# Performance work log

Measured on AMD Instinct MI355X. Metric: run time of the kernel, lower is better.

Reference implementation:

```python
import jax, jax.numpy as jnp
import numpy as np

# Winograd F(2x2, 3x3) transform matrices, copied verbatim from the source
# (note: G[1,2] is 1.2 in the original code, not 0.5 -- replicated faithfully).
B_MAT = jnp.array([[1, 0, -1, 0], [0, 1, 1, 0], [0, -1, 1, 0], [0, 1, 0, -1]], dtype=jnp.float32)
G_MAT = jnp.array([[1.0, 0.0, 0.0], [0.5, 0.5, 1.2], [0.5, -0.5, 0.5], [0.0, 0.0, 1.0]], dtype=jnp.float32)
AT_MAT = jnp.array([[1, 1, 1, 0], [0, 1, -1, -1]], dtype=jnp.float32)


def setup_inputs() -> dict:
    key = jax.random.key(0)
    k1, k2 = jax.random.split(key)
    x = jax.random.normal(k1, (64, 64, 64, 64), dtype=jnp.float32)        # [B, C, H, W]
    filters = jax.random.normal(k2, (64, 64, 3, 3), dtype=jnp.float32)    # [F, C, 3, 3]
    return {"x": x, "filters": filters}


def winograd_forward(x, filters):
    bs, C, H, W = x.shape
    F = filters.shape[0]
    m, r = 2, 3
    alpha = m + r - 1          # 4
    over = r - 1               # 2 (tile stride)
    T = (W - alpha) // over + 1
    p = bs * T * T

    # U[f,c] = G @ g @ G^T   -> [F, C, 4, 4]
    U = jnp.einsum('ij,fcjk,lk->fcil', G_MAT, filters, G_MAT)

    # Extract all 4x4 input tiles with stride 2: [C, B, T, T, 4, 4]
    xt = jnp.transpose(x, (1, 0, 2, 3))                         # [C, B, H, W]
    win = (jnp.arange(T) * over)[:, None] + jnp.arange(alpha)[None, :]  # [T, 4]
    patches = xt[:, :, win[:, None, :, None], win[None, :, None, :]]    # [C,B,T,T,4,4]

    # V[c,b] = B^T @ d @ B, flattened with b = batch*T*T + row*T + col
    V = jnp.einsum('ji,cbtujk,kl->cbtuil', B_MAT, patches, B_MAT)
    V = V.reshape(C, p, alpha, alpha)

    # Faithful to the source bug: M[f, j] is only accumulated for j < T
    # (the loop is `for j in range(tiles)` instead of range(p)); rest stay zero.
    Mpart = jnp.einsum('fcab,cjab->fjab', U, V[:, :T])          # [F, T, 4, 4]
    M = jnp.zeros((F, p, alpha, alpha), x.dtype).at[:, :T].set(Mpart)

    # Faithful to the source: Y tile index b = f*T*T + k*T + l (depends on the
    # filter index, not the batch index), so every batch gets the same tiles.
    idx = (jnp.arange(F) * T * T)[:, None] + jnp.arange(T * T)[None, :]  # [F, T*T]
    Msel = M[jnp.arange(F)[:, None], idx]                        # [F, T*T, 4, 4]

    # Inverse transform: A^T @ M @ A -> [F, T*T, 2, 2]
    Yt = jnp.einsum('ij,ftjk,kl->ftil', AT_MAT, Msel, AT_MAT.T)
    out_h = H - r + 1
    Yt = Yt.reshape(F, T, T, m, m).transpose(0, 1, 3, 2, 4).reshape(F, T * m, T * m)
    # Original allocates Y as [F, B, H-2, H-2]; with H == W they match T*m.
    Y = jnp.broadcast_to(Yt[:, None, :, :], (F, bs, out_h, out_h))
    return jnp.transpose(Y, (1, 0, 2, 3))                        # [B, F, H-2, H-2]


def reference(x, filters):
    return winograd_forward(x, filters)
```

## Files before the change

### kernel.cpp

```cpp
#include <hip/hip_runtime.h>


__global__ void winograd_scatter(const float* __restrict__ x,
                                 const float* __restrict__ filters,
                                 float* __restrict__ out) {
    const int u = blockIdx.x;
    const int c = threadIdx.x;

    const float G[4][3]  = {{1.0f, 0.0f, 0.0f},
                            {0.5f, 0.5f, 1.2f},
                            {0.5f,-0.5f, 0.5f},
                            {0.0f, 0.0f, 1.0f}};
    const float Bm[4][4] = {{1.f, 0.f,-1.f, 0.f},
                            {0.f, 1.f, 1.f, 0.f},
                            {0.f,-1.f, 1.f, 0.f},
                            {0.f, 1.f, 0.f,-1.f}};

    float g[3][3];
#pragma unroll
    for (int j = 0; j < 3; ++j)
#pragma unroll
        for (int k = 0; k < 3; ++k)
            g[j][k] = filters[c * 9 + j * 3 + k];

    float t1[4][3];
#pragma unroll
    for (int i = 0; i < 4; ++i)
#pragma unroll
        for (int k = 0; k < 3; ++k) {
            float s = 0.f;
#pragma unroll
            for (int j = 0; j < 3; ++j) s += G[i][j] * g[j][k];
            t1[i][k] = s;
        }
    float U[4][4];
#pragma unroll
    for (int i = 0; i < 4; ++i)
#pragma unroll
        for (int l = 0; l < 4; ++l) {
            float s = 0.f;
#pragma unroll
            for (int k = 0; k < 3; ++k) s += t1[i][k] * G[l][k];
            U[i][l] = s;
        }

    float d[4][4];
#pragma unroll
    for (int j = 0; j < 4; ++j)
#pragma unroll
        for (int k = 0; k < 4; ++k)
            d[j][k] = x[c * 4096 + j * 64 + 2 * u + k];

    float t2[4][4];
#pragma unroll
    for (int i = 0; i < 4; ++i)
#pragma unroll
        for (int k = 0; k < 4; ++k) {
            float s = 0.f;
#pragma unroll
            for (int j = 0; j < 4; ++j) s += Bm[j][i] * d[j][k];
            t2[i][k] = s;
        }
    float V[4][4];
#pragma unroll
    for (int i = 0; i < 4; ++i)
#pragma unroll
        for (int l = 0; l < 4; ++l) {
            float s = 0.f;
#pragma unroll
            for (int k = 0; k < 4; ++k) s += t2[i][k] * Bm[k][l];
            V[i][l] = s;
        }

    __shared__ float red[16][64];
#pragma unroll
    for (int i = 0; i < 4; ++i)
#pragma unroll
        for (int l = 0; l < 4; ++l)
            red[i * 4 + l][c] = U[i][l] * V[i][l];
    __syncthreads();

    __shared__ float M[16];
    if (c < 16) {
        float s = 0.f;
        for (int t = 0; t < 64; ++t) s += red[c][t];
        M[c] = s;
    }
    __syncthreads();

    __shared__ float sY[4];
    if (c == 0) {
        const float AT[2][4] = {{1.f, 1.f, 1.f, 0.f},
                                {0.f, 1.f,-1.f,-1.f}};
        float t3[2][4];
#pragma unroll
        for (int i = 0; i < 2; ++i)
#pragma unroll
            for (int k = 0; k < 4; ++k) {
                float s = 0.f;
#pragma unroll
                for (int j = 0; j < 4; ++j) s += AT[i][j] * M[j * 4 + k];
                t3[i][k] = s;
            }
#pragma unroll
        for (int i = 0; i < 2; ++i)
#pragma unroll
            for (int l = 0; l < 2; ++l) {
                float s = 0.f;
#pragma unroll
                for (int k = 0; k < 4; ++k) s += t3[i][k] * AT[l][k];
                sY[i * 2 + l] = s;
            }
    }
    __syncthreads();

    const float2 r0 = make_float2(sY[0], sY[1]);
    const float2 r1 = make_float2(sY[2], sY[3]);
    float* base = out + (size_t)c * 246016 + 2 * u;
    *(float2*)(base)      = r0;
    *(float2*)(base + 62) = r1;
}

extern "C" void kernel_launch(void* const* d_in, const int* in_sizes, int n_in,
                              void* d_out, int out_size, void* d_ws, size_t ws_size,
                              hipStream_t stream) {
    const float* x       = (const float*)d_in[0];
    const float* filters = (const float*)d_in[1];
    float* out = (float*)d_out;

    hipMemsetAsync(d_out, 0, (size_t)out_size * sizeof(float), stream);
    winograd_scatter<<<31, 64, 0, stream>>>(x, filters, out);
}
```

Measured before the change: 105.6 us.

## Fuse output zero-fill into compute kernel, drop separate memset

```diff
diff --git a/kernel.cpp b/kernel.cpp
--- a/kernel.cpp
+++ b/kernel.cpp
@@ -1,95 +1,119 @@
 #include <hip/hip_runtime.h>
 
 
-__global__ void winograd_scatter(const float* __restrict__ x,
-                                 const float* __restrict__ filters,
-                                 float* __restrict__ out) {
+#define COMPUTE_BLOCKS 31
+#define FILL_BLOCKS    2048
+#define BLOCK          256
+#define N4             3936256
+#define BSTRIDE4       61504
+#define SKIP4          31
+
+__global__ __launch_bounds__(BLOCK)
+void winograd_fused(const float* __restrict__ x,
+                    const float* __restrict__ filters,
+                    float* __restrict__ out) {
+    const int tid = threadIdx.x;
+
+    if (blockIdx.x >= COMPUTE_BLOCKS) {
+        const int fb = (int)blockIdx.x - COMPUTE_BLOCKS;
+        const float4 z = make_float4(0.f, 0.f, 0.f, 0.f);
+        float4* __restrict__ o4 = (float4*)out;
+        for (int i = fb * BLOCK + tid; i < N4; i += FILL_BLOCKS * BLOCK) {
+            const int rem = i % BSTRIDE4;
+            if (rem >= SKIP4) o4[i] = z;
+        }
+        return;
+    }
+
     const int u = blockIdx.x;
-    const int c = threadIdx.x;
-
-    const float G[4][3]  = {{1.0f, 0.0f, 0.0f},
-                            {0.5f, 0.5f, 1.2f},
-                            {0.5f,-0.5f, 0.5f},
-                            {0.0f, 0.0f, 1.0f}};
-    const float Bm[4][4] = {{1.f, 0.f,-1.f, 0.f},
-                            {0.f, 1.f, 1.f, 0.f},
-                            {0.f,-1.f, 1.f, 0.f},
-                            {0.f, 1.f, 0.f,-1.f}};
-
-    float g[3][3];
-#pragma unroll
-    for (int j = 0; j < 3; ++j)
-#pragma unroll
-        for (int k = 0; k < 3; ++k)
-            g[j][k] = filters[c * 9 + j * 3 + k];
-
-    float t1[4][3];
-#pragma unroll
-    for (int i = 0; i < 4; ++i)
-#pragma unroll
-        for (int k = 0; k < 3; ++k) {
-            float s = 0.f;
-#pragma unroll
-            for (int j = 0; j < 3; ++j) s += G[i][j] * g[j][k];
-            t1[i][k] = s;
-        }
-    float U[4][4];
-#pragma unroll
-    for (int i = 0; i < 4; ++i)
-#pragma unroll
-        for (int l = 0; l < 4; ++l) {
-            float s = 0.f;
-#pragma unroll
-            for (int k = 0; k < 3; ++k) s += t1[i][k] * G[l][k];
-            U[i][l] = s;
-        }
-
-    float d[4][4];
-#pragma unroll
-    for (int j = 0; j < 4; ++j)
-#pragma unroll
-        for (int k = 0; k < 4; ++k)
-            d[j][k] = x[c * 4096 + j * 64 + 2 * u + k];
-
-    float t2[4][4];
-#pragma unroll
-    for (int i = 0; i < 4; ++i)
-#pragma unroll
-        for (int k = 0; k < 4; ++k) {
-            float s = 0.f;
-#pragma unroll
-            for (int j = 0; j < 4; ++j) s += Bm[j][i] * d[j][k];
-            t2[i][k] = s;
-        }
-    float V[4][4];
-#pragma unroll
-    for (int i = 0; i < 4; ++i)
-#pragma unroll
-        for (int l = 0; l < 4; ++l) {
-            float s = 0.f;
-#pragma unroll
-            for (int k = 0; k < 4; ++k) s += t2[i][k] * Bm[k][l];
-            V[i][l] = s;
-        }
+    const int c = tid & 63;
 
     __shared__ float red[16][64];
+    __shared__ float Msm[16];
+    __shared__ float sY[4];
+
+    if (tid < 64) {
+        const float G[4][3]  = {{1.0f, 0.0f, 0.0f},
+                                {0.5f, 0.5f, 1.2f},
+                                {0.5f,-0.5f, 0.5f},
+                                {0.0f, 0.0f, 1.0f}};
+        const float Bm[4][4] = {{1.f, 0.f,-1.f, 0.f},
+                                {0.f, 1.f, 1.f, 0.f},
+                                {0.f,-1.f, 1.f, 0.f},
+                                {0.f, 1.f, 0.f,-1.f}};
+
+        float g[3][3];
 #pragma unroll
-    for (int i = 0; i < 4; ++i)
+        for (int j = 0; j < 3; ++j)
 #pragma unroll
-        for (int l = 0; l < 4; ++l)
-            red[i * 4 + l][c] = U[i][l] * V[i][l];
-    __syncthreads();
+            for (int k = 0; k < 3; ++k)
+                g[j][k] = filters[c * 9 + j * 3 + k];
 
-    __shared__ float M[16];
-    if (c < 16) {
-        float s = 0.f;
-        for (int t = 0; t < 64; ++t) s += red[c][t];
-        M[c] = s;
+        float t1[4][3];
+#pragma unroll
+        for (int i = 0; i < 4; ++i)
+#pragma unroll
+            for (int k = 0; k < 3; ++k) {
+                float s = 0.f;
+#pragma unroll
+                for (int j = 0; j < 3; ++j) s += G[i][j] * g[j][k];
+                t1[i][k] = s;
+            }
+        float U[4][4];
+#pragma unroll
+        for (int i = 0; i < 4; ++i)
+#pragma unroll
+            for (int l = 0; l < 4; ++l) {
+                float s = 0.f;
+#pragma unroll
+                for (int k = 0; k < 3; ++k) s += t1[i][k] * G[l][k];
+                U[i][l] = s;
+            }
+
+        float d[4][4];
+#pragma unroll
+        for (int j = 0; j < 4; ++j)
+#pragma unroll
+            for (int k = 0; k < 4; ++k)
+                d[j][k] = x[c * 4096 + j * 64 + 2 * u + k];
+
+        float t2[4][4];
+#pragma unroll
+        for (int i = 0; i < 4; ++i)
+#pragma unroll
+            for (int k = 0; k < 4; ++k) {
+                float s = 0.f;
+#pragma unroll
+                for (int j = 0; j < 4; ++j) s += Bm[j][i] * d[j][k];
+                t2[i][k] = s;
+            }
+        float V[4][4];
+#pragma unroll
+        for (int i = 0; i < 4; ++i)
+#pragma unroll
+            for (int l = 0; l < 4; ++l) {
+                float s = 0.f;
+#pragma unroll
+                for (int k = 0; k < 4; ++k) s += t2[i][k] * Bm[k][l];
+                V[i][l] = s;
+            }
+
+#pragma unroll
+        for (int i = 0; i < 4; ++i)
+#pragma unroll
+            for (int l = 0; l < 4; ++l)
+                red[i * 4 + l][c] = U[i][l] * V[i][l];
     }
     __syncthreads();
 
-    __shared__ float sY[4];
-    if (c == 0) {
+    if (tid < 16) {
+        float s = 0.f;
+        for (int t = 0; t < 64; ++t) s += red[tid][t];
+        Msm[tid] = s;
+    }
+    __syncthreads();
+
+    if (tid == 0) {
         const float AT[2][4] = {{1.f, 1.f, 1.f, 0.f},
                                 {0.f, 1.f,-1.f,-1.f}};
         float t3[2][4];
@@ -99,7 +123,7 @@
             for (int k = 0; k < 4; ++k) {
                 float s = 0.f;
 #pragma unroll
-                for (int j = 0; j < 4; ++j) s += AT[i][j] * M[j * 4 + k];
+                for (int j = 0; j < 4; ++j) s += AT[i][j] * Msm[j * 4 + k];
                 t3[i][k] = s;
             }
 #pragma unroll
@@ -114,11 +138,13 @@
     }
     __syncthreads();
 
-    const float2 r0 = make_float2(sY[0], sY[1]);
-    const float2 r1 = make_float2(sY[2], sY[3]);
-    float* base = out + (size_t)c * 246016 + 2 * u;
-    *(float2*)(base)      = r0;
-    *(float2*)(base + 62) = r1;
+    if (tid < 64) {
+        const float2 r0 = make_float2(sY[0], sY[1]);
+        const float2 r1 = make_float2(sY[2], sY[3]);
+        float* base = out + (size_t)c * 246016 + 2 * u;
+        *(float2*)(base)      = r0;
+        *(float2*)(base + 62) = r1;
+    }
 }
 
 extern "C" void kernel_launch(void* const* d_in, const int* in_sizes, int n_in,
@@ -128,6 +154,5 @@
     const float* filters = (const float*)d_in[1];
     float* out = (float*)d_out;
 
-    hipMemsetAsync(d_out, 0, (size_t)out_size * sizeof(float), stream);
-    winograd_scatter<<<31, 64, 0, stream>>>(x, filters, out);
+    winograd_fused<<<COMPUTE_BLOCKS + FILL_BLOCKS, BLOCK, 0, stream>>>(x, filters, out);
 }
```

Measured after the change: 101.0 us. -4.3%, faster.
